# Performance work log

Hardware: AMD Instinct MI355X
Metric: run time of the kernel (lower is better)

The kernel has to match this reference:

```python
import jax, jax.numpy as jnp
import numpy as np

N_NODES = 50000
N_EDGES = 800000


def setup_inputs() -> dict:
    key = jax.random.key(0)
    k_h, k_e, k_w1, k_w2 = jax.random.split(key, 4)
    d_in, d_hid, d_out = 128, 128, 128
    h = jax.random.normal(k_h, (N_NODES, d_in), dtype=jnp.float32)
    edge_index = jax.random.randint(k_e, (2, N_EDGES), 0, N_NODES, dtype=jnp.int64)
    # Linear weights ~ PyTorch default scale
    W1 = jax.random.normal(k_w1, (d_hid, d_in), dtype=jnp.float32) * (1.0 / np.sqrt(d_in))
    b1 = jnp.zeros((d_hid,), dtype=jnp.float32)
    W2 = jax.random.normal(k_w2, (d_out, d_hid), dtype=jnp.float32) * (1.0 / np.sqrt(d_hid))
    b2 = jnp.zeros((d_out,), dtype=jnp.float32)
    return {"h": h, "edge_index": edge_index, "W1": W1, "b1": b1, "W2": W2, "b2": b2}


def _sage_gcn(h, src, dst, W, b):
    # DGL SAGEConv with 'gcn' aggregator (eval mode):
    #   h_neigh = (segment_sum(h[src] -> dst) + h) / (in_deg + 1)
    #   out     = h_neigh @ W^T + b   (only fc_neigh is used for 'gcn')
    n = h.shape[0]
    agg = jax.ops.segment_sum(h[src], dst, num_segments=n)          # [N, d]
    deg = jax.ops.segment_sum(jnp.ones_like(dst, dtype=h.dtype), dst, num_segments=n)  # [N]
    h_neigh = (agg + h) / (deg[:, None] + 1.0)
    return h_neigh @ W.T + b


def reference(h, edge_index, W1, b1, W2, b2):
    src, dst = edge_index[0], edge_index[1]
    # Layer 1 + ReLU (dropout inactive in eval mode)
    h1 = jax.nn.relu(_sage_gcn(h, src, dst, W1, b1))
    # Layer 2 (no activation on final layer)
    return _sage_gcn(h1, src, dst, W2, b2)
```

## Files before the change

kernel.cpp:

```cpp
#include <hip/hip_runtime.h>

typedef unsigned short ushort_t;
typedef __attribute__((ext_vector_type(8))) short short8;
typedef __attribute__((ext_vector_type(8))) unsigned short ushort8;
typedef __attribute__((ext_vector_type(8))) __bf16 bf16x8;
typedef __attribute__((ext_vector_type(4))) float f32x4;

#define N_NODES 50000
#define N_EDGES 800000
#define D 128
#define N4 (N_NODES / 4)
#define BSTRIDE 64
#define NBIN 8
#define BIN_DIV 6250
#define BIN_CAP 112640
#define BIN_BLOCKS ((N_EDGES + 1023) / 1024)
#define SC_BPB ((BIN_CAP + 255) / 256)

#define XB_B    0
#define XB1_B   12800000
#define WBHI1_B 25600000
#define WBLO1_B 25632768
#define WBHI2_B 25665536
#define WBLO2_B 25698304
#define CNT_B   25731072
#define CSR_B   25931104

__device__ __forceinline__ ushort_t f2bf(float f) {
    unsigned u = __builtin_bit_cast(unsigned, f);
    return (ushort_t)((u + 0x7FFFu + ((u >> 16) & 1u)) >> 16);
}
__device__ __forceinline__ float bf2f(ushort_t b) {
    return __builtin_bit_cast(float, ((unsigned)b) << 16);
}

__device__ __forceinline__ f32x4 mfma16(short8 a, short8 b, f32x4 c) {
    return __builtin_amdgcn_mfma_f32_16x16x32_bf16(
        __builtin_bit_cast(bf16x8, a), __builtin_bit_cast(bf16x8, b), c, 0, 0, 0);
}

__device__ __forceinline__ int wfrag_off(int k, int j) {
    int nt = j >> 4;
    int kt = k >> 5;
    int lane = (((k >> 3) & 3) << 4) | (j & 15);
    int i = k & 7;
    return ((nt * 4 + kt) << 9) + (lane << 3) + i;
}

__global__ __launch_bounds__(256) void init_kernel(const float* __restrict__ h,
                                                   const float* __restrict__ W1,
                                                   const float* __restrict__ W2,
                                                   ushort_t* __restrict__ wbhi1,
                                                   ushort_t* __restrict__ wblo1,
                                                   ushort_t* __restrict__ wbhi2,
                                                   ushort_t* __restrict__ wblo2,
                                                   ushort_t* __restrict__ xb,
                                                   int* __restrict__ cnt) {
    int idx = blockIdx.x * 256 + threadIdx.x;
    if (idx < N4 + 2) {
        ((int4*)cnt)[idx] = make_int4(0, 0, 0, 0);
        return;
    }
    int i = idx - (N4 + 2);
    if (i < D * D) {
        int j = i >> 7;
        int k = i & 127;
        int off = wfrag_off(k, j);
        float w1 = W1[i];
        ushort_t h1 = f2bf(w1);
        wbhi1[off] = h1;
        wblo1[off] = f2bf(w1 - bf2f(h1));
        float w2 = W2[i];
        ushort_t h2 = f2bf(w2);
        wbhi2[off] = h2;
        wblo2[off] = f2bf(w2 - bf2f(h2));
        return;
    }
    int j = i - D * D;
    if (j < N_NODES * D / 4) {
        float4 v = ((const float4*)h)[j];
        ushort4 o;
        o.x = f2bf(v.x); o.y = f2bf(v.y); o.z = f2bf(v.z); o.w = f2bf(v.w);
        ((ushort4*)xb)[j] = o;
    }
}

__global__ __launch_bounds__(256) void bin_kernel(const int* __restrict__ src,
                                                  const int* __restrict__ dst,
                                                  int* __restrict__ bincur,
                                                  unsigned* __restrict__ binbuf) {
    __shared__ int cnts[NBIN];
    __shared__ int base[NBIN];
    int t = threadIdx.x;
    if (t < NBIN) cnts[t] = 0;
    __syncthreads();
    unsigned pk[4];
    int bn[4];
    int ofs[4];
    int e0 = blockIdx.x * 1024 + t;
#pragma unroll
    for (int i = 0; i < 4; ++i) {
        int e = e0 + i * 256;
        bn[i] = -1;
        if (e < N_EDGES) {
            int s = src[e];
            int d = dst[e];
            pk[i] = (unsigned)s | ((unsigned)d << 16);
            bn[i] = d / BIN_DIV;
            ofs[i] = atomicAdd(&cnts[bn[i]], 1);
        }
    }
    __syncthreads();
    if (t < NBIN) base[t] = atomicAdd(&bincur[t], cnts[t]);
    __syncthreads();
#pragma unroll
    for (int i = 0; i < 4; ++i) {
        if (bn[i] >= 0) {
            int pos = base[bn[i]] + ofs[i];
            if (pos < BIN_CAP) binbuf[(size_t)bn[i] * BIN_CAP + pos] = pk[i];
        }
    }
}

__global__ __launch_bounds__(256) void scatter2_kernel(const unsigned* __restrict__ binbuf,
                                                       const int* __restrict__ bincur,
                                                       int* __restrict__ cnt,
                                                       ushort_t* __restrict__ csr) {
    int bin = blockIdx.x & 7;
    int chunk = blockIdx.x >> 3;
    int n = bincur[bin];
    if (n > BIN_CAP) n = BIN_CAP;
    int i = chunk * 256 + threadIdx.x;
    if (i < n) {
        unsigned pk = binbuf[(size_t)bin * BIN_CAP + i];
        int s = (int)(pk & 0xFFFFu);
        int d = (int)(pk >> 16);
        int p = atomicAdd(&cnt[d], 1);
        if (p < BSTRIDE) csr[(size_t)d * BSTRIDE + p] = (ushort_t)s;
    }
}

template <int RELU, int OUTBF16>
__global__ __launch_bounds__(256, 6) void sage_fused_kernel(const ushort_t* __restrict__ xb,
                                                            const int* __restrict__ cnt,
                                                            const ushort_t* __restrict__ csr,
                                                            const ushort_t* __restrict__ wbhi,
                                                            const ushort_t* __restrict__ wblo,
                                                            const float* __restrict__ bias,
                                                            void* __restrict__ outp) {
    __shared__ ushort_t xl[32 * 136];
    const int t = threadIdx.x;
    const int n0 = blockIdx.x * 32;
    const int gg = t >> 4;
    const int cl = t & 15;
    const ushort8* xb8 = (const ushort8*)xb;

#pragma unroll
    for (int q = 0; q < 2; ++q) {
        int n = gg * 2 + q;
        int node = n0 + n;
        float acc[8];
        if (node < N_NODES) {
            ushort8 sv = xb8[(size_t)node * 16 + cl];
#pragma unroll
            for (int j = 0; j < 8; ++j) acc[j] = bf2f(sv[j]);
            int deg = cnt[node];
            if (deg > BSTRIDE) deg = BSTRIDE;
            const ushort_t* row = csr + (size_t)node * BSTRIDE;
            int i = 0;
            for (; i + 8 <= deg; i += 8) {
                ushort8 v[8];
#pragma unroll
                for (int u = 0; u < 8; ++u) {
                    int s = (int)row[i + u];
                    v[u] = xb8[(size_t)s * 16 + cl];
                }
#pragma unroll
                for (int u = 0; u < 8; ++u) {
#pragma unroll
                    for (int j = 0; j < 8; ++j) acc[j] += bf2f(v[u][j]);
                }
            }
            if (i + 4 <= deg) {
                ushort8 v[4];
#pragma unroll
                for (int u = 0; u < 4; ++u) {
                    int s = (int)row[i + u];
                    v[u] = xb8[(size_t)s * 16 + cl];
                }
#pragma unroll
                for (int u = 0; u < 4; ++u) {
#pragma unroll
                    for (int j = 0; j < 8; ++j) acc[j] += bf2f(v[u][j]);
                }
                i += 4;
            }
            for (; i < deg; ++i) {
                int s = (int)row[i];
                ushort8 v = xb8[(size_t)s * 16 + cl];
#pragma unroll
                for (int j = 0; j < 8; ++j) acc[j] += bf2f(v[j]);
            }
            float iv = 1.0f / (float)(deg + 1);
#pragma unroll
            for (int j = 0; j < 8; ++j) acc[j] *= iv;
        } else {
#pragma unroll
            for (int j = 0; j < 8; ++j) acc[j] = 0.f;
        }
        ushort8 o;
#pragma unroll
        for (int j = 0; j < 8; ++j) o[j] = f2bf(acc[j]);
        *(ushort8*)(&xl[n * 136 + cl * 8]) = o;
    }

    __syncthreads();

    const int w = t >> 6;
    const int l = t & 63;
    const int lr = l & 15;
    const int lg = l >> 4;
    const short8* bh = (const short8*)wbhi;
    const short8* bl = (const short8*)wblo;

    float b0 = bias[(2 * w) * 16 + lr];
    float b1 = bias[(2 * w + 1) * 16 + lr];
    f32x4 acc[2][2];
    acc[0][0] = (f32x4){b0, b0, b0, b0};
    acc[1][0] = (f32x4){b0, b0, b0, b0};
    acc[0][1] = (f32x4){b1, b1, b1, b1};
    acc[1][1] = (f32x4){b1, b1, b1, b1};

#pragma unroll
    for (int kt = 0; kt < 4; ++kt) {
        short8 a0 = *(const short8*)(&xl[lr * 136 + kt * 32 + lg * 8]);
        short8 a1 = *(const short8*)(&xl[(16 + lr) * 136 + kt * 32 + lg * 8]);
        short8 b0h = bh[((2 * w) * 4 + kt) * 64 + l];
        short8 b0l = bl[((2 * w) * 4 + kt) * 64 + l];
        short8 b1h = bh[((2 * w + 1) * 4 + kt) * 64 + l];
        short8 b1l = bl[((2 * w + 1) * 4 + kt) * 64 + l];
        acc[0][0] = mfma16(a0, b0h, acc[0][0]);
        acc[0][0] = mfma16(a0, b0l, acc[0][0]);
        acc[1][0] = mfma16(a1, b0h, acc[1][0]);
        acc[1][0] = mfma16(a1, b0l, acc[1][0]);
        acc[0][1] = mfma16(a0, b1h, acc[0][1]);
        acc[0][1] = mfma16(a0, b1l, acc[0][1]);
        acc[1][1] = mfma16(a1, b1h, acc[1][1]);
        acc[1][1] = mfma16(a1, b1l, acc[1][1]);
    }

#pragma unroll
    for (int mt = 0; mt < 2; ++mt) {
#pragma unroll
        for (int nn = 0; nn < 2; ++nn) {
            int col = (2 * w + nn) * 16 + lr;
#pragma unroll
            for (int r = 0; r < 4; ++r) {
                int node = n0 + mt * 16 + lg * 4 + r;
                if (node >= N_NODES) continue;
                float v = acc[mt][nn][r];
                if (RELU) v = fmaxf(v, 0.f);
                if (OUTBF16) {
                    ((ushort_t*)outp)[(size_t)node * 128 + col] = f2bf(v);
                } else {
                    ((float*)outp)[(size_t)node * 128 + col] = v;
                }
            }
        }
    }
}

extern "C" void kernel_launch(void* const* d_in, const int* in_sizes, int n_in,
                              void* d_out, int out_size, void* d_ws, size_t ws_size,
                              hipStream_t stream) {
    const float* h  = (const float*)d_in[0];
    const int*   ei = (const int*)d_in[1];
    const float* W1 = (const float*)d_in[2];
    const float* b1 = (const float*)d_in[3];
    const float* W2 = (const float*)d_in[4];
    const float* b2 = (const float*)d_in[5];
    char* ws = (char*)d_ws;

    ushort_t* xb    = (ushort_t*)(ws + XB_B);
    ushort_t* xb1   = (ushort_t*)(ws + XB1_B);
    unsigned* binbuf = (unsigned*)(ws + XB1_B);
    ushort_t* wbhi1 = (ushort_t*)(ws + WBHI1_B);
    ushort_t* wblo1 = (ushort_t*)(ws + WBLO1_B);
    ushort_t* wbhi2 = (ushort_t*)(ws + WBHI2_B);
    ushort_t* wblo2 = (ushort_t*)(ws + WBLO2_B);
    int* cnt        = (int*)(ws + CNT_B);
    int* bincur     = cnt + N_NODES;
    ushort_t* csr   = (ushort_t*)(ws + CSR_B);

    const int* src = ei;
    const int* dst = ei + N_EDGES;

    int init_threads = (N4 + 2) + D * D + N_NODES * D / 4;
    init_kernel<<<(init_threads + 255) / 256, 256, 0, stream>>>(h, W1, W2, wbhi1, wblo1, wbhi2, wblo2, xb, cnt);
    bin_kernel<<<BIN_BLOCKS, 256, 0, stream>>>(src, dst, bincur, binbuf);
    scatter2_kernel<<<NBIN * SC_BPB, 256, 0, stream>>>(binbuf, bincur, cnt, csr);

    sage_fused_kernel<1, 1><<<(N_NODES + 31) / 32, 256, 0, stream>>>(xb, cnt, csr, wbhi1, wblo1, b1, (void*)xb1);
    sage_fused_kernel<0, 0><<<(N_NODES + 31) / 32, 256, 0, stream>>>(xb1, cnt, csr, wbhi2, wblo2, b2, d_out);
}
```

Baseline: 127.1 us.

## Build compact CSR via 80-bin partition and per-bin counting sort

```diff
diff --git a/kernel.cpp b/kernel.cpp
--- a/kernel.cpp
+++ b/kernel.cpp
@@ -9,13 +9,10 @@
 #define N_NODES 50000
 #define N_EDGES 800000
 #define D 128
-#define N4 (N_NODES / 4)
-#define BSTRIDE 64
-#define NBIN 8
-#define BIN_DIV 6250
-#define BIN_CAP 112640
+#define NB80 80
+#define B80_DIV 625
+#define B80_CAP 12032
 #define BIN_BLOCKS ((N_EDGES + 1023) / 1024)
-#define SC_BPB ((BIN_CAP + 255) / 256)
 
 #define XB_B    0
 #define XB1_B   12800000
@@ -23,8 +20,9 @@
 #define WBLO1_B 25632768
 #define WBHI2_B 25665536
 #define WBLO2_B 25698304
-#define CNT_B   25731072
-#define CSR_B   25931104
+#define RS_B    25731072
+#define BC80_B  25931088
+#define CSR_B   25931408
 
 __device__ __forceinline__ ushort_t f2bf(float f) {
     unsigned u = __builtin_bit_cast(unsigned, f);
@@ -55,13 +53,13 @@
                                                    ushort_t* __restrict__ wbhi2,
                                                    ushort_t* __restrict__ wblo2,
                                                    ushort_t* __restrict__ xb,
-                                                   int* __restrict__ cnt) {
+                                                   int* __restrict__ bincur) {
     int idx = blockIdx.x * 256 + threadIdx.x;
-    if (idx < N4 + 2) {
-        ((int4*)cnt)[idx] = make_int4(0, 0, 0, 0);
+    if (idx < 20) {
+        ((int4*)bincur)[idx] = make_int4(0, 0, 0, 0);
         return;
     }
-    int i = idx - (N4 + 2);
+    int i = idx - 20;
     if (i < D * D) {
         int j = i >> 7;
         int k = i & 127;
@@ -85,14 +83,14 @@
     }
 }
 
-__global__ __launch_bounds__(256) void bin_kernel(const int* __restrict__ src,
-                                                  const int* __restrict__ dst,
-                                                  int* __restrict__ bincur,
-                                                  unsigned* __restrict__ binbuf) {
-    __shared__ int cnts[NBIN];
-    __shared__ int base[NBIN];
+__global__ __launch_bounds__(256) void bin80_kernel(const int* __restrict__ src,
+                                                    const int* __restrict__ dst,
+                                                    int* __restrict__ bincur,
+                                                    unsigned* __restrict__ binbuf) {
+    __shared__ int cnts[NB80];
+    __shared__ int base[NB80];
     int t = threadIdx.x;
-    if (t < NBIN) cnts[t] = 0;
+    if (t < NB80) cnts[t] = 0;
     __syncthreads();
     unsigned pk[4];
     int bn[4];
@@ -106,43 +104,93 @@
             int s = src[e];
             int d = dst[e];
             pk[i] = (unsigned)s | ((unsigned)d << 16);
-            bn[i] = d / BIN_DIV;
+            bn[i] = d / B80_DIV;
             ofs[i] = atomicAdd(&cnts[bn[i]], 1);
         }
     }
     __syncthreads();
-    if (t < NBIN) base[t] = atomicAdd(&bincur[t], cnts[t]);
+    if (t < NB80) base[t] = atomicAdd(&bincur[t], cnts[t]);
     __syncthreads();
 #pragma unroll
     for (int i = 0; i < 4; ++i) {
         if (bn[i] >= 0) {
             int pos = base[bn[i]] + ofs[i];
-            if (pos < BIN_CAP) binbuf[(size_t)bn[i] * BIN_CAP + pos] = pk[i];
-        }
-    }
-}
-
-__global__ __launch_bounds__(256) void scatter2_kernel(const unsigned* __restrict__ binbuf,
-                                                       const int* __restrict__ bincur,
-                                                       int* __restrict__ cnt,
-                                                       ushort_t* __restrict__ csr) {
-    int bin = blockIdx.x & 7;
-    int chunk = blockIdx.x >> 3;
-    int n = bincur[bin];
-    if (n > BIN_CAP) n = BIN_CAP;
-    int i = chunk * 256 + threadIdx.x;
-    if (i < n) {
-        unsigned pk = binbuf[(size_t)bin * BIN_CAP + i];
-        int s = (int)(pk & 0xFFFFu);
-        int d = (int)(pk >> 16);
-        int p = atomicAdd(&cnt[d], 1);
-        if (p < BSTRIDE) csr[(size_t)d * BSTRIDE + p] = (ushort_t)s;
+            if (pos < B80_CAP) binbuf[(size_t)bn[i] * B80_CAP + pos] = pk[i];
+        }
+    }
+}
+
+__global__ __launch_bounds__(256) void sort_kernel(const unsigned* __restrict__ binbuf,
+                                                   const int* __restrict__ bincur,
+                                                   int* __restrict__ row_start,
+                                                   ushort_t* __restrict__ csr) {
+    __shared__ int hist[B80_DIV];
+    __shared__ int psum[B80_DIV];
+    __shared__ int carry[16];
+    __shared__ int baseS;
+    const int t = threadIdx.x;
+    const int sb = blockIdx.x;
+    const int d0 = sb * B80_DIV;
+    if (t == 0) {
+        int b = 0;
+        for (int j = 0; j < sb; ++j) b += bincur[j];
+        baseS = b;
+    }
+    for (int k = t; k < B80_DIV; k += 256) hist[k] = 0;
+    __syncthreads();
+    int n = bincur[sb];
+    if (n > B80_CAP) n = B80_CAP;
+    const unsigned* seg = binbuf + (size_t)sb * B80_CAP;
+    for (int i = t; i < n; i += 256) {
+        int d = (int)(seg[i] >> 16) - d0;
+        atomicAdd(&hist[d], 1);
+    }
+    __syncthreads();
+    for (int k = t; k < B80_DIV; k += 256) psum[k] = hist[k];
+    __syncthreads();
+    {
+        int lane = t & 63, wv = t >> 6;
+        for (int ch = wv; ch < 10; ch += 4) {
+            int idx = ch * 64 + lane;
+            int v = (idx < B80_DIV) ? psum[idx] : 0;
+#pragma unroll
+            for (int off = 1; off < 64; off <<= 1) {
+                int u = __shfl_up(v, off, 64);
+                if (lane >= off) v += u;
+            }
+            if (idx < B80_DIV) psum[idx] = v;
+        }
+    }
+    __syncthreads();
+    if (t == 0) {
+        int c = 0;
+        for (int ch = 0; ch < 10; ++ch) {
+            carry[ch] = c;
+            int last = ch * 64 + 63;
+            if (last >= B80_DIV) last = B80_DIV - 1;
+            c += psum[last];
+        }
+    }
+    __syncthreads();
+    const int base = baseS;
+    for (int k = t; k < B80_DIV; k += 256) {
+        int excl = carry[k >> 6] + psum[k] - hist[k];
+        row_start[d0 + k] = base + excl;
+        hist[k] = excl;
+    }
+    if (sb == NB80 - 1 && t == 0) row_start[N_NODES] = base + n;
+    __syncthreads();
+    for (int i = t; i < n; i += 256) {
+        unsigned pk = seg[i];
+        int d = (int)(pk >> 16) - d0;
+        int slot = atomicAdd(&hist[d], 1);
+        csr[base + slot] = (ushort_t)(pk & 0xFFFFu);
     }
 }
 
 template <int RELU, int OUTBF16>
 __global__ __launch_bounds__(256, 6) void sage_fused_kernel(const ushort_t* __restrict__ xb,
-                                                            const int* __restrict__ cnt,
+                                                            const int* __restrict__ row_start,
                                                             const ushort_t* __restrict__ csr,
                                                             const ushort_t* __restrict__ wbhi,
                                                             const ushort_t* __restrict__ wblo,
@@ -164,9 +212,10 @@
             ushort8 sv = xb8[(size_t)node * 16 + cl];
 #pragma unroll
             for (int j = 0; j < 8; ++j) acc[j] = bf2f(sv[j]);
-            int deg = cnt[node];
-            if (deg > BSTRIDE) deg = BSTRIDE;
-            const ushort_t* row = csr + (size_t)node * BSTRIDE;
+            int e0 = row_start[node];
+            int e1 = row_start[node + 1];
+            int deg = e1 - e0;
+            const ushort_t* row = csr + e0;
             int i = 0;
             for (; i + 8 <= deg; i += 8) {
                 ushort8 v[8];
@@ -281,25 +330,25 @@
     const float* b2 = (const float*)d_in[5];
     char* ws = (char*)d_ws;
 
-    ushort_t* xb    = (ushort_t*)(ws + XB_B);
-    ushort_t* xb1   = (ushort_t*)(ws + XB1_B);
+    ushort_t* xb     = (ushort_t*)(ws + XB_B);
+    ushort_t* xb1    = (ushort_t*)(ws + XB1_B);
     unsigned* binbuf = (unsigned*)(ws + XB1_B);
-    ushort_t* wbhi1 = (ushort_t*)(ws + WBHI1_B);
-    ushort_t* wblo1 = (ushort_t*)(ws + WBLO1_B);
-    ushort_t* wbhi2 = (ushort_t*)(ws + WBHI2_B);
-    ushort_t* wblo2 = (ushort_t*)(ws + WBLO2_B);
-    int* cnt        = (int*)(ws + CNT_B);
-    int* bincur     = cnt + N_NODES;
-    ushort_t* csr   = (ushort_t*)(ws + CSR_B);
+    ushort_t* wbhi1  = (ushort_t*)(ws + WBHI1_B);
+    ushort_t* wblo1  = (ushort_t*)(ws + WBLO1_B);
+    ushort_t* wbhi2  = (ushort_t*)(ws + WBHI2_B);
+    ushort_t* wblo2  = (ushort_t*)(ws + WBLO2_B);
+    int* row_start   = (int*)(ws + RS_B);
+    int* bincur      = (int*)(ws + BC80_B);
+    ushort_t* csr    = (ushort_t*)(ws + CSR_B);
 
     const int* src = ei;
     const int* dst = ei + N_EDGES;
 
-    int init_threads = (N4 + 2) + D * D + N_NODES * D / 4;
-    init_kernel<<<(init_threads + 255) / 256, 256, 0, stream>>>(h, W1, W2, wbhi1, wblo1, wbhi2, wblo2, xb, cnt);
-    bin_kernel<<<BIN_BLOCKS, 256, 0, stream>>>(src, dst, bincur, binbuf);
-    scatter2_kernel<<<NBIN * SC_BPB, 256, 0, stream>>>(binbuf, bincur, cnt, csr);
-
-    sage_fused_kernel<1, 1><<<(N_NODES + 31) / 32, 256, 0, stream>>>(xb, cnt, csr, wbhi1, wblo1, b1, (void*)xb1);
-    sage_fused_kernel<0, 0><<<(N_NODES + 31) / 32, 256, 0, stream>>>(xb1, cnt, csr, wbhi2, wblo2, b2, d_out);
-}
+    int init_threads = 20 + D * D + N_NODES * D / 4;
+    init_kernel<<<(init_threads + 255) / 256, 256, 0, stream>>>(h, W1, W2, wbhi1, wblo1, wbhi2, wblo2, xb, bincur);
+    bin80_kernel<<<BIN_BLOCKS, 256, 0, stream>>>(src, dst, bincur, binbuf);
+    sort_kernel<<<NB80, 256, 0, stream>>>(binbuf, bincur, row_start, csr);
+
+    sage_fused_kernel<1, 1><<<(N_NODES + 31) / 32, 256, 0, stream>>>(xb, row_start, csr, wbhi1, wblo1, b1, (void*)xb1);
+    sage_fused_kernel<0, 0><<<(N_NODES + 31) / 32, 256, 0, stream>>>(xb1, row_start, csr, wbhi2, wblo2, b2, d_out);
+}
```

Measured after the change: 127.1 us. No clear change (-0.0%).
